# Kernel tuning notes

Measured on AMD Instinct MI355X. Metric: run time of the kernel, lower is better.

The kernel has to match this reference:

```python
import jax, jax.numpy as jnp
import numpy as np

CHUNK = 2048  # i-tile size; each block kernel slab is CHUNK x M (128 MB fp32), never the full N x M


def setup_inputs() -> dict:
    key = jax.random.key(0)
    k1, k2, k3, k4 = jax.random.split(key, 4)
    ls = jax.random.uniform(k1, (1,), dtype=jnp.float32)          # scalar lengthscale g (Pm(0,1))
    x = jax.random.normal(k2, (16384, 32), dtype=jnp.float32)     # Vi points
    y = jax.random.normal(k3, (16384, 32), dtype=jnp.float32)     # Vj points
    b = jax.random.normal(k4, (16384, 16), dtype=jnp.float32)     # Vj RHS
    return {"ls": ls, "x": x, "y": y, "b": b}


def reference(ls, x, y, b):
    # out[i] = sum_j exp(-g * ||x_i - y_j||^2) * b[j]   (KeOps Genred Sum over axis=1)
    g = ls[0]
    N, D = x.shape
    yn = jnp.sum(y * y, axis=1)  # [M]

    def blk(xc):  # xc: [CHUNK, D]
        xn = jnp.sum(xc * xc, axis=1, keepdims=True)                   # [CHUNK, 1]
        sq = jnp.maximum(xn + yn[None, :] - 2.0 * (xc @ y.T), 0.0)     # [CHUNK, M]
        return jnp.exp(-g * sq) @ b                                    # [CHUNK, Dv]

    out = jax.lax.map(blk, x.reshape(N // CHUNK, CHUNK, D))
    return out.reshape(N, b.shape[1])
```

## Files before the change

kernel.cpp:

```cpp
#include <hip/hip_runtime.h>


#define NPTS 16384
#define D    32
#define DV   16
#define IBLK 256
#define JSPLIT 16
#define JBLK 64
#define NTILE  (NPTS / JBLK)
#define TILES  (NTILE / JSPLIT)
#define REC    12800
#define YH_OFF 256
#define YL_OFF 5376
#define BT_OFF 10496
#define PTS    72
#define PART_F4 (NPTS * DV / 4)

typedef _Float16 half8   __attribute__((ext_vector_type(8)));
typedef __fp16   cvt2_t  __attribute__((ext_vector_type(2)));
typedef float    float4_t __attribute__((ext_vector_type(4)));
typedef unsigned int u32;
typedef unsigned int u32x2 __attribute__((ext_vector_type(2)));

__device__ __forceinline__ void async16(const void* g, void* l) {
  __builtin_amdgcn_global_load_lds((const __attribute__((address_space(1))) u32*)g,
                                   (__attribute__((address_space(3))) u32*)l, 16, 0, 0);
}

__device__ __forceinline__ void stage_tile(const char* __restrict__ g,
                                           char* __restrict__ l, int tid) {
  async16(g + tid * 16,         l + tid * 16);
  async16(g + 4096 + tid * 16,  l + 4096 + tid * 16);
  async16(g + 8192 + tid * 16,  l + 8192 + tid * 16);
  if (tid < 32) async16(g + 12288 + tid * 16, l + 12288 + tid * 16);
}

__device__ __forceinline__ void permswap32(u32& a, u32& b) {
#if __has_builtin(__builtin_amdgcn_permlane32_swap)
  u32x2 r = __builtin_amdgcn_permlane32_swap(a, b, false, false);
  a = r[0]; b = r[1];
#else
  asm("v_permlane32_swap_b32 %0, %1" : "+v"(a), "+v"(b));
#endif
}

__device__ __forceinline__ void permswap16(u32& a, u32& b) {
#if __has_builtin(__builtin_amdgcn_permlane16_swap)
  u32x2 r = __builtin_amdgcn_permlane16_swap(a, b, false, false);
  a = r[0]; b = r[1];
#else
  asm("v_permlane16_swap_b32 %0, %1" : "+v"(a), "+v"(b));
#endif
}

__global__ __launch_bounds__(64) void rbf_prologue(
    const float* __restrict__ ls, const float* __restrict__ y,
    const float* __restrict__ b, char* __restrict__ rec0,
    float* __restrict__ outz, int zero_out) {
  __shared__ _Float16 sbt[64][17];
  const int tid = threadIdx.x;
  const int tt  = blockIdx.x;
  const int j   = tt * 64 + tid;
  char* rec = rec0 + (size_t)tt * REC;
  const float nl2g = -ls[0] * 1.4426950408889634f;

  const float4* yp = (const float4*)(y + (size_t)j * D);
  float s = 0.f;
  _Float16 hi[32], lo[32];
  #pragma unroll
  for (int c = 0; c < 8; ++c) {
    float4 v = yp[c];
    float f[4] = {v.x, v.y, v.z, v.w};
    #pragma unroll
    for (int k = 0; k < 4; ++k) {
      s = fmaf(f[k], f[k], s);
      _Float16 h = (_Float16)f[k];
      hi[c*4+k] = h;
      lo[c*4+k] = (_Float16)(f[k] - (float)h);
    }
  }
  ((float*)rec)[tid] = nl2g * s;
  #pragma unroll
  for (int c = 0; c < 4; ++c) {
    *(half8*)(rec + YH_OFF + tid * 80 + c * 16) = *(half8*)&hi[c*8];
    *(half8*)(rec + YL_OFF + tid * 80 + c * 16) = *(half8*)&lo[c*8];
  }

  const float4* bp = (const float4*)(b + (size_t)j * DV);
  #pragma unroll
  for (int c = 0; c < 4; ++c) {
    float4 v = bp[c];
    sbt[tid][c*4+0] = (_Float16)v.x; sbt[tid][c*4+1] = (_Float16)v.y;
    sbt[tid][c*4+2] = (_Float16)v.z; sbt[tid][c*4+3] = (_Float16)v.w;
  }
  __syncthreads();
  #pragma unroll
  for (int r = 0; r < 2; ++r) {
    int cch = r * 64 + tid;
    int v = cch >> 3, jg = cch & 7;
    _Float16 tmp[8];
    #pragma unroll
    for (int k = 0; k < 8; ++k) tmp[k] = sbt[jg*8 + k][v];
    *(half8*)(rec + BT_OFF + v*144 + jg*16) = *(half8*)tmp;
  }

  if (zero_out) {
    float4 z = {0.f, 0.f, 0.f, 0.f};
    float4* ozp = (float4*)outz;
    #pragma unroll
    for (int r = 0; r < 4; ++r) ozp[blockIdx.x * 256 + r * 64 + tid] = z;
  }
}

template <int MODE>
__global__ __launch_bounds__(256, 4) void rbf_mfma(
    const float* __restrict__ ls, const float* __restrict__ x,
    const char* __restrict__ rec0, float* __restrict__ out,
    float* __restrict__ part) {
  __shared__ __align__(16) char SB[2][REC];

  const int tid  = threadIdx.x;
  const int lane = tid & 63, w = tid >> 6;
  const int t = lane & 15, q = lane >> 4;
  const int xcd = blockIdx.x & 7, rr = blockIdx.x >> 3;
  const int jseg = xcd * 2 + (rr & 1);
  const int iblk = rr >> 1;
  const int tseg = jseg * TILES;

  const float nl2g = -ls[0] * 1.4426950408889634f;
  const float m2g  = -2.0f * nl2g;

  half8 xh[4], xl[4];
  float xns[4];
  #pragma unroll
  for (int f = 0; f < 4; ++f) {
    const int row = iblk * IBLK + f * 64 + w * 16 + t;
    const float4* xp = (const float4*)(x + (size_t)row * D + q * 8);
    float4 a0 = xp[0], a1 = xp[1];
    float fv[8] = {a0.x,a0.y,a0.z,a0.w,a1.x,a1.y,a1.z,a1.w};
    float s = 0.f;
    #pragma unroll
    for (int k = 0; k < 8; ++k) {
      s = fmaf(fv[k], fv[k], s);
      float vv = m2g * fv[k];
      _Float16 h = (_Float16)vv;
      xh[f][k] = h;
      xl[f][k] = (_Float16)(vv - (float)h);
    }
    s += __shfl_xor(s, 16);
    s += __shfl_xor(s, 32);
    xns[f] = fmaf(nl2g, s, 14.0f);
  }

  float4_t acc[4] = {{0,0,0,0},{0,0,0,0},{0,0,0,0},{0,0,0,0}};

  stage_tile(rec0 + (size_t)tseg * REC, &SB[0][0], tid);
  __syncthreads();

  for (int k = 0; k < TILES; ++k) {
    if (k + 1 < TILES)
      stage_tile(rec0 + (size_t)(tseg + k + 1) * REC, &SB[(k + 1) & 1][0], tid);

    const char* rec = &SB[k & 1][0];
    const float* ynp = (const float*)rec;
    const char* yhp = rec + YH_OFF;
    const char* ylp = rec + YL_OFF;
    const _Float16* btp = (const _Float16*)(rec + BT_OFF);

    half8 ah[4], al[4];
    float4_t yn4[4];
    #pragma unroll
    for (int s = 0; s < 4; ++s) {
      ah[s]  = *(const half8*)(yhp + (s * 16 + t) * 80 + q * 16);
      al[s]  = *(const half8*)(ylp + (s * 16 + t) * 80 + q * 16);
      yn4[s] = *(const float4_t*)(ynp + s * 16 + q * 4);
    }
    const half8 bh0 = *(const half8*)(btp + t * PTS + q * 8);
    const half8 bh1 = *(const half8*)(btp + t * PTS + 32 + q * 8);

    #pragma unroll
    for (int f = 0; f < 4; ++f) {
      const float4_t xns4 = {xns[f], xns[f], xns[f], xns[f]};
      u32 S[4][2];
      #pragma unroll
      for (int s = 0; s < 4; ++s) {
        float4_t e = yn4[s] + xns4;
        e = __builtin_amdgcn_mfma_f32_16x16x32_f16(ah[s], xh[f], e, 0, 0, 0);
        e = __builtin_amdgcn_mfma_f32_16x16x32_f16(ah[s], xl[f], e, 0, 0, 0);
        e = __builtin_amdgcn_mfma_f32_16x16x32_f16(al[s], xh[f], e, 0, 0, 0);
        float p0 = __builtin_amdgcn_exp2f(e[0]);
        float p1 = __builtin_amdgcn_exp2f(e[1]);
        float p2 = __builtin_amdgcn_exp2f(e[2]);
        float p3 = __builtin_amdgcn_exp2f(e[3]);
        union { cvt2_t c2; u32 u; } w0, w1;
        w0.c2 = __builtin_amdgcn_cvt_pkrtz(p0, p1);
        w1.c2 = __builtin_amdgcn_cvt_pkrtz(p2, p3);
        S[s][0] = w0.u; S[s][1] = w1.u;
      }
      u32 t0[4], t1[4];
      #pragma unroll
      for (int r = 0; r < 2; ++r) {
        u32 a = S[0][r], b = S[1][r];
        permswap32(a, b); permswap16(a, b);
        t0[r] = a; t0[2 + r] = b;
        a = S[2][r]; b = S[3][r];
        permswap32(a, b); permswap16(a, b);
        t1[r] = a; t1[2 + r] = b;
      }
      union { u32 u[4]; half8 h; } up0, up1;
      up0.u[0] = t0[0]; up0.u[1] = t0[1]; up0.u[2] = t0[2]; up0.u[3] = t0[3];
      up1.u[0] = t1[0]; up1.u[1] = t1[1]; up1.u[2] = t1[2]; up1.u[3] = t1[3];
      acc[f] = __builtin_amdgcn_mfma_f32_16x16x32_f16(bh0, up0.h, acc[f], 0, 0, 0);
      acc[f] = __builtin_amdgcn_mfma_f32_16x16x32_f16(bh1, up1.h, acc[f], 0, 0, 0);
    }
    __syncthreads();
  }

  #pragma unroll
  for (int f = 0; f < 4; ++f) {
    const int row = iblk * IBLK + f * 64 + w * 16 + t;
    if (MODE == 0) {
      const float sc = 0.00006103515625f;
      float* orow = out + (size_t)row * DV + q * 4;
      #pragma unroll
      for (int r = 0; r < 4; ++r) atomicAdd(&orow[r], acc[f][r] * sc);
    } else {
      *(float4_t*)(part + ((size_t)jseg * NPTS + row) * DV + q * 4) = acc[f];
    }
  }
}

__global__ __launch_bounds__(256) void rbf_reduce(
    const float4_t* __restrict__ part, float4_t* __restrict__ out) {
  const int i = blockIdx.x * 256 + threadIdx.x;
  float4_t s = part[i];
  #pragma unroll
  for (int k = 1; k < JSPLIT; ++k) s += part[(size_t)k * PART_F4 + i];
  out[i] = s * 0.00006103515625f;
}

#define BJ     128
#define BLOCK  256
#define FJSPLIT 32
#define SYP    36

__global__ __launch_bounds__(BLOCK) void rbf_fp32_kernel(
    const float* __restrict__ ls, const float* __restrict__ x,
    const float* __restrict__ y, const float* __restrict__ b,
    float* __restrict__ out, int N, int M) {
  __shared__ float sy[BJ * SYP];
  __shared__ float sb[BJ * DV];
  __shared__ float syn[BJ];
  const int itiles = N / BLOCK;
  const int itile  = blockIdx.x & (itiles - 1);
  const int jseg   = blockIdx.x / itiles;
  const int i      = itile * BLOCK + threadIdx.x;
  const int jlen   = M / FJSPLIT;
  const int j0     = jseg * jlen;
  const float g    = ls[0];
  const float nl2g = -g * 1.4426950408889634f;
  float xr[D]; float xn = 0.f;
  {
    const float4* xp = (const float4*)(x + (size_t)i * D);
    #pragma unroll
    for (int qq = 0; qq < D / 4; ++qq) {
      float4 v = xp[qq];
      xr[4*qq+0]=v.x; xr[4*qq+1]=v.y; xr[4*qq+2]=v.z; xr[4*qq+3]=v.w;
      xn += v.x*v.x + v.y*v.y + v.z*v.z + v.w*v.w;
    }
  }
  float acc[DV];
  #pragma unroll
  for (int v = 0; v < DV; ++v) acc[v] = 0.f;
  for (int jt = j0; jt < j0 + jlen; jt += BJ) {
    {
      const float4* src = (const float4*)(y + (size_t)jt * D);
      #pragma unroll
      for (int r = 0; r < (BJ * D / 4) / BLOCK; ++r) {
        int e4 = r * BLOCK + threadIdx.x;
        int j  = e4 >> 3; int dq = e4 & 7;
        *(float4*)&sy[j * SYP + dq * 4] = src[e4];
      }
      const float4* bsrc = (const float4*)(b + (size_t)jt * DV);
      #pragma unroll
      for (int r = 0; r < (BJ * DV / 4) / BLOCK; ++r) {
        int e4 = r * BLOCK + threadIdx.x;
        *(float4*)&sb[e4 * 4] = bsrc[e4];
      }
    }
    __syncthreads();
    if (threadIdx.x < BJ) {
      const float* row = &sy[threadIdx.x * SYP];
      float s0=0,s1=0,s2=0,s3=0;
      #pragma unroll
      for (int d = 0; d < D; d += 4) {
        s0=fmaf(row[d+0],row[d+0],s0); s1=fmaf(row[d+1],row[d+1],s1);
        s2=fmaf(row[d+2],row[d+2],s2); s3=fmaf(row[d+3],row[d+3],s3);
      }
      syn[threadIdx.x] = (s0+s1)+(s2+s3);
    }
    __syncthreads();
    #pragma unroll 2
    for (int j = 0; j < BJ; ++j) {
      const float* yrow = &sy[j * SYP];
      float d0=0,d1=0,d2=0,d3=0;
      #pragma unroll
      for (int d = 0; d < D; d += 4) {
        d0=fmaf(xr[d+0],yrow[d+0],d0); d1=fmaf(xr[d+1],yrow[d+1],d1);
        d2=fmaf(xr[d+2],yrow[d+2],d2); d3=fmaf(xr[d+3],yrow[d+3],d3);
      }
      float dot=(d0+d1)+(d2+d3);
      float sq = fmaxf(xn + syn[j] - 2.0f*dot, 0.0f);
      float p  = exp2f(nl2g * sq);
      const float* brow = &sb[j * DV];
      #pragma unroll
      for (int v = 0; v < DV; ++v) acc[v] = fmaf(p, brow[v], acc[v]);
    }
    __syncthreads();
  }
  float* orow = out + (size_t)i * DV;
  #pragma unroll
  for (int v = 0; v < DV; ++v) atomicAdd(&orow[v], acc[v]);
}

extern "C" void kernel_launch(void* const* d_in, const int* in_sizes, int n_in,
                              void* d_out, int out_size, void* d_ws, size_t ws_size,
                              hipStream_t stream) {
  const float* ls = (const float*)d_in[0];
  const float* x  = (const float*)d_in[1];
  const float* y  = (const float*)d_in[2];
  const float* b  = (const float*)d_in[3];
  float* out = (float*)d_out;

  const size_t need_rec  = (size_t)NTILE * REC;
  const size_t need_part = need_rec + (size_t)JSPLIT * NPTS * DV * 4;

  if (ws_size >= need_part) {
    char* rec0 = (char*)d_ws;
    float* part = (float*)(rec0 + need_rec);
    rbf_prologue<<<NTILE, 64, 0, stream>>>(ls, y, b, rec0, out, 0);
    dim3 grid((NPTS / IBLK) * JSPLIT);
    rbf_mfma<1><<<grid, 256, 0, stream>>>(ls, x, rec0, out, part);
    rbf_reduce<<<PART_F4 / 256, 256, 0, stream>>>((const float4_t*)part,
                                                  (float4_t*)out);
  } else if (ws_size >= need_rec) {
    char* rec0 = (char*)d_ws;
    rbf_prologue<<<NTILE, 64, 0, stream>>>(ls, y, b, rec0, out, 1);
    dim3 grid((NPTS / IBLK) * JSPLIT);
    rbf_mfma<0><<<grid, 256, 0, stream>>>(ls, x, rec0, out, nullptr);
  } else {
    (void)hipMemsetAsync(d_out, 0, (size_t)out_size * sizeof(float), stream);
    dim3 grid((NPTS / BLOCK) * FJSPLIT);
    rbf_fp32_kernel<<<grid, BLOCK, 0, stream>>>(ls, x, y, b, out, NPTS, NPTS);
  }
}
```

Before: 136.0 us.

## Fuse split-J partial reduction into MFMA kernel via last-block counter

Removes the separate reduce kernel launch. Each i-block now keeps an atomic counter, reset in the prologue, and whichever of the JSPLIT blocks finishes last sums the partial slabs and writes the output. This saves a kernel launch and its gap, at the cost of threadfences, an atomic per block and a serialized tail reduction done by only 64 blocks.

```diff
diff --git a/kernel.cpp b/kernel.cpp
--- a/kernel.cpp
+++ b/kernel.cpp
@@ -56,7 +56,7 @@
 __global__ __launch_bounds__(64) void rbf_prologue(
     const float* __restrict__ ls, const float* __restrict__ y,
     const float* __restrict__ b, char* __restrict__ rec0,
-    float* __restrict__ outz, int zero_out) {
+    float* __restrict__ outz, int zero_out, u32* __restrict__ cnt) {
   __shared__ _Float16 sbt[64][17];
   const int tid = threadIdx.x;
   const int tt  = blockIdx.x;
@@ -64,6 +64,8 @@
   char* rec = rec0 + (size_t)tt * REC;
   const float nl2g = -ls[0] * 1.4426950408889634f;
 
+  if (cnt && tid == 0 && tt < 64) cnt[tt] = 0;
+
   const float4* yp = (const float4*)(y + (size_t)j * D);
   float s = 0.f;
   _Float16 hi[32], lo[32];
@@ -116,8 +118,9 @@
 __global__ __launch_bounds__(256, 4) void rbf_mfma(
     const float* __restrict__ ls, const float* __restrict__ x,
     const char* __restrict__ rec0, float* __restrict__ out,
-    float* __restrict__ part) {
+    float* __restrict__ part, u32* __restrict__ cnt) {
   __shared__ __align__(16) char SB[2][REC];
+  __shared__ int lastflag;
 
   const int tid  = threadIdx.x;
   const int lane = tid & 63, w = tid >> 6;
@@ -216,27 +219,43 @@
     __syncthreads();
   }
 
-  #pragma unroll
-  for (int f = 0; f < 4; ++f) {
-    const int row = iblk * IBLK + f * 64 + w * 16 + t;
-    if (MODE == 0) {
+  if (MODE == 0) {
+    #pragma unroll
+    for (int f = 0; f < 4; ++f) {
+      const int row = iblk * IBLK + f * 64 + w * 16 + t;
       const float sc = 0.00006103515625f;
       float* orow = out + (size_t)row * DV + q * 4;
       #pragma unroll
       for (int r = 0; r < 4; ++r) atomicAdd(&orow[r], acc[f][r] * sc);
-    } else {
+    }
+  } else {
+    #pragma unroll
+    for (int f = 0; f < 4; ++f) {
+      const int row = iblk * IBLK + f * 64 + w * 16 + t;
       *(float4_t*)(part + ((size_t)jseg * NPTS + row) * DV + q * 4) = acc[f];
     }
-  }
-}
-
-__global__ __launch_bounds__(256) void rbf_reduce(
-    const float4_t* __restrict__ part, float4_t* __restrict__ out) {
-  const int i = blockIdx.x * 256 + threadIdx.x;
-  float4_t s = part[i];
-  #pragma unroll
-  for (int k = 1; k < JSPLIT; ++k) s += part[(size_t)k * PART_F4 + i];
-  out[i] = s * 0.00006103515625f;
+    __threadfence();
+    if (tid == 0) {
+      u32 prev = atomicAdd(&cnt[iblk], 1u);
+      lastflag = (prev == (u32)(JSPLIT - 1));
+    }
+    __syncthreads();
+    if (lastflag) {
+      __threadfence();
+      const float4_t* pp = (const float4_t*)part;
+      float4_t* op = (float4_t*)out;
+      #pragma unroll
+      for (int r = 0; r < 4; ++r) {
+        const int idx = r * 256 + tid;
+        const size_t base = (size_t)iblk * 1024 + idx;
+        float4_t s = pp[base];
+        #pragma unroll 4
+        for (int k2 = 1; k2 < JSPLIT; ++k2)
+          s += pp[(size_t)k2 * PART_F4 + base];
+        op[base] = s * 0.00006103515625f;
+      }
+    }
+  }
 }
 
 #define BJ     128
@@ -333,21 +352,21 @@
   float* out = (float*)d_out;
 
   const size_t need_rec  = (size_t)NTILE * REC;
-  const size_t need_part = need_rec + (size_t)JSPLIT * NPTS * DV * 4;
+  const size_t slabs     = (size_t)JSPLIT * NPTS * DV * 4;
+  const size_t need_part = need_rec + slabs + 256;
 
   if (ws_size >= need_part) {
     char* rec0 = (char*)d_ws;
     float* part = (float*)(rec0 + need_rec);
-    rbf_prologue<<<NTILE, 64, 0, stream>>>(ls, y, b, rec0, out, 0);
+    u32* cnt = (u32*)(rec0 + need_rec + slabs);
+    rbf_prologue<<<NTILE, 64, 0, stream>>>(ls, y, b, rec0, out, 0, cnt);
     dim3 grid((NPTS / IBLK) * JSPLIT);
-    rbf_mfma<1><<<grid, 256, 0, stream>>>(ls, x, rec0, out, part);
-    rbf_reduce<<<PART_F4 / 256, 256, 0, stream>>>((const float4_t*)part,
-                                                  (float4_t*)out);
+    rbf_mfma<1><<<grid, 256, 0, stream>>>(ls, x, rec0, out, part, cnt);
   } else if (ws_size >= need_rec) {
     char* rec0 = (char*)d_ws;
-    rbf_prologue<<<NTILE, 64, 0, stream>>>(ls, y, b, rec0, out, 1);
+    rbf_prologue<<<NTILE, 64, 0, stream>>>(ls, y, b, rec0, out, 1, nullptr);
     dim3 grid((NPTS / IBLK) * JSPLIT);
-    rbf_mfma<0><<<grid, 256, 0, stream>>>(ls, x, rec0, out, nullptr);
+    rbf_mfma<0><<<grid, 256, 0, stream>>>(ls, x, rec0, out, nullptr, nullptr);
   } else {
     (void)hipMemsetAsync(d_out, 0, (size_t)out_size * sizeof(float), stream);
     dim3 grid((NPTS / BLOCK) * FJSPLIT);
```

Result: slower. 327.9 us (+141.1%).
